# Performance work log

Hardware: AMD Instinct MI355X
Metric: run time of the kernel (lower is better)

The kernel has to match this reference:

```python
import jax, jax.numpy as jnp
import numpy as np

NUM_HEADS = 12

def rel_indices(N):
    # [N, N, 3] = (dx, dy, dist^2) between patches on an img x img grid
    img = int(N ** 0.5)
    ind = jnp.arange(img)[None, :] - jnp.arange(img)[:, None]      # [img, img]
    indx = jnp.tile(ind, (img, img))                               # [N, N]
    indy = jnp.repeat(jnp.repeat(ind, img, axis=0), img, axis=1)   # [N, N]
    indd = indx ** 2 + indy ** 2
    return jnp.stack([indx, indy, indd], axis=-1).astype(jnp.float32)

def setup_inputs() -> dict:
    key = jax.random.key(0)
    ks = jax.random.split(key, 8)
    B, N, C, H = 16, 576, 768, NUM_HEADS
    std = 0.02  # trunc_normal init scale in the original
    return {
        "x": jax.random.normal(ks[0], (B, N, C), jnp.float32),
        "w_qk": jax.random.normal(ks[1], (C, 2 * C), jnp.float32) * std,
        "w_v": jax.random.normal(ks[2], (C, C), jnp.float32) * std,
        "w_proj": jax.random.normal(ks[3], (C, C), jnp.float32) * std,
        "b_proj": jnp.zeros((C,), jnp.float32),
        "w_pos": jax.random.normal(ks[4], (3, H), jnp.float32) * std,
        "b_pos": jnp.zeros((H,), jnp.float32),
        "gating": jnp.ones((H,), jnp.float32),
    }

def reference(x, w_qk, w_v, w_proj, b_proj, w_pos, b_pos, gating):
    B, N, C = x.shape
    H = NUM_HEADS
    Dh = C // H
    scale = Dh ** -0.5

    # q, k: [B, H, N, Dh]
    qk = (x @ w_qk).reshape(B, N, 2, H, Dh)
    q = jnp.transpose(qk[:, :, 0], (0, 2, 1, 3))
    k = jnp.transpose(qk[:, :, 1], (0, 2, 1, 3))

    # content scores, softmax over keys
    patch_score = jax.nn.softmax(
        jnp.einsum("bhnd,bhmd->bhnm", q, k) * scale, axis=-1)

    # positional scores: rel_indices [N,N,3] -> [H,N,N], softmax over keys
    rel = rel_indices(N)
    pos_logits = jnp.einsum("nmk,kh->hnm", rel, w_pos) + b_pos[:, None, None]
    pos_score = jax.nn.softmax(pos_logits, axis=-1)  # [H, N, N]

    # sigmoid gating + renormalization
    g = jax.nn.sigmoid(gating)[None, :, None, None]
    attn = (1.0 - g) * patch_score + g * pos_score[None]
    attn = attn / jnp.sum(attn, axis=-1, keepdims=True)

    # v: [B, H, N, Dh]
    v = jnp.transpose((x @ w_v).reshape(B, N, H, Dh), (0, 2, 1, 3))

    out = jnp.einsum("bhnm,bhmd->bnhd", attn, v).reshape(B, N, C)
    out = out @ w_proj + b_proj
    return (out, attn, v)
```

## Files before the change

kernel.cpp:

```cpp
#include <hip/hip_runtime.h>
#include <hip/hip_bf16.h>

typedef __bf16 bf16;
typedef __attribute__((ext_vector_type(4))) __bf16 bf16x4;
typedef __attribute__((ext_vector_type(8))) __bf16 bf16x8;
typedef __attribute__((ext_vector_type(4))) float floatx4;

#define BB 16
#define NN 576
#define CC 768
#define HH 12
#define DH 64

#define GLOAD_LDS16(gp, lp) __builtin_amdgcn_global_load_lds( \
    (const __attribute__((address_space(1))) unsigned int*)(const void*)(gp), \
    (__attribute__((address_space(3))) unsigned int*)(void*)(lp), 16, 0, 0)

__global__ void k_convert(const float* __restrict__ in, bf16* __restrict__ out, int n4){
  int i = blockIdx.x*blockDim.x + threadIdx.x;
  if (i < n4){
    float4 f = ((const float4*)in)[i];
    bf16x4 o;
    o[0]=(bf16)f.x; o[1]=(bf16)f.y; o[2]=(bf16)f.z; o[3]=(bf16)f.w;
    ((bf16x4*)out)[i] = o;
  }
}

__global__ void k_transpose(const float* __restrict__ src, bf16* __restrict__ dst, int R, int Cc){
  __shared__ float tile[32][33];
  int c0 = blockIdx.x*32, r0 = blockIdx.y*32;
  int tx = threadIdx.x & 31, ty = threadIdx.x >> 5;
  #pragma unroll
  for (int i=0;i<4;i++)
    tile[ty + i*8][tx] = src[(size_t)(r0 + ty + i*8)*Cc + c0 + tx];
  __syncthreads();
  #pragma unroll
  for (int i=0;i<4;i++)
    dst[(size_t)(c0 + ty + i*8)*R + r0 + tx] = (bf16)tile[tx][ty + i*8];
}

__global__ __launch_bounds__(256) void k_pos(const float* __restrict__ w_pos, bf16* __restrict__ pos){
  int t = threadIdx.x, wv = t>>6, lane = t&63;
  int rowid = blockIdx.x*4 + wv;
  int h = rowid / NN, n = rowid % NN;
  float w0 = w_pos[h], w1 = w_pos[HH + h], w2 = w_pos[2*HH + h];
  int nx = n % 24, ny = n / 24;
  float e[9]; float mx = -1e30f;
  #pragma unroll
  for (int j=0;j<9;j++){
    int idx = lane + 64*j;
    int qq = idx / 144;
    int r  = idx - qq*144;
    int m  = (r>>2)*16 + qq*4 + (r&3);
    float dx = (float)(m % 24 - nx);
    float dy = (float)(m / 24 - ny);
    float l = dx*w0 + dy*w1 + (dx*dx + dy*dy)*w2;
    e[j] = l; mx = fmaxf(mx, l);
  }
  #pragma unroll
  for (int s=1;s<64;s<<=1) mx = fmaxf(mx, __shfl_xor(mx, s, 64));
  float sum = 0.f;
  #pragma unroll
  for (int j=0;j<9;j++){ e[j] = __expf(e[j]-mx); sum += e[j]; }
  #pragma unroll
  for (int s=1;s<64;s<<=1) sum += __shfl_xor(sum, s, 64);
  float inv = 1.f/sum;
  bf16* dst = pos + (size_t)rowid*NN;
  #pragma unroll
  for (int j=0;j<9;j++) dst[lane + 64*j] = (bf16)(e[j]*inv);
}

__device__ __forceinline__ void gemm128_main(
    const bf16* __restrict__ A, const bf16* __restrict__ B,
    int lda, int ldb, int K, bf16* As, bf16* Bs, floatx4 (*acc)[4])
{
  int t = threadIdx.x;
  int w = t>>6, m16 = t&15, q = (t&63)>>4;
  int wr = (w>>1)*64, wc = (w&1)*64;
  int sr = t>>2, kg = (t&3)*8;
  bf16* ldsA = As + w*512;
  bf16* ldsB = Bs + w*512;
  for (int k0 = 0; k0 < K; k0 += 32){
    GLOAD_LDS16(A + (size_t)sr*lda      + k0 + kg, ldsA);
    GLOAD_LDS16(A + (size_t)(sr+64)*lda + k0 + kg, ldsA + 2048);
    GLOAD_LDS16(B + (size_t)sr*ldb      + k0 + kg, ldsB);
    GLOAD_LDS16(B + (size_t)(sr+64)*ldb + k0 + kg, ldsB + 2048);
    __syncthreads();
    bf16x8 af[4], bfv[4];
    #pragma unroll
    for (int rt=0;rt<4;rt++) af[rt]  = *(const bf16x8*)&As[(wr + rt*16 + m16)*32 + q*8];
    #pragma unroll
    for (int ct=0;ct<4;ct++) bfv[ct] = *(const bf16x8*)&Bs[(wc + ct*16 + m16)*32 + q*8];
    #pragma unroll
    for (int rt=0;rt<4;rt++)
      #pragma unroll
      for (int ct=0;ct<4;ct++)
        acc[rt][ct] = __builtin_amdgcn_mfma_f32_16x16x32_bf16(af[rt], bfv[ct], acc[rt][ct], 0, 0, 0);
    __syncthreads();
  }
}

__global__ __launch_bounds__(256) void k_gemm1(
    const bf16* __restrict__ x_bf, const bf16* __restrict__ wcatT,
    bf16* __restrict__ q_bf, bf16* __restrict__ k_bf,
    bf16* __restrict__ vt_bf, float* __restrict__ v_out)
{
  __shared__ bf16 As[128*32];
  __shared__ bf16 Bs[128*32];
  int cb = blockIdx.x % 18, rb = blockIdx.x / 18;
  int rowBase = rb*128, colBase = cb*128;
  floatx4 zero = {0.f,0.f,0.f,0.f};
  floatx4 acc[4][4];
  #pragma unroll
  for (int a=0;a<4;a++)
    #pragma unroll
    for (int b=0;b<4;b++) acc[a][b] = zero;
  gemm128_main(x_bf + (size_t)rowBase*CC, wcatT + (size_t)colBase*CC, CC, CC, CC, As, Bs, acc);
  int t = threadIdx.x;
  int w = t>>6, m16 = t&15, q = (t&63)>>4;
  int wr = (w>>1)*64, wc = (w&1)*64;
  #pragma unroll
  for (int rt=0;rt<4;rt++){
    #pragma unroll
    for (int i=0;i<4;i++){
      int row = rowBase + wr + rt*16 + q*4 + i;
      int b = row / NN, n = row % NN;
      #pragma unroll
      for (int ct=0;ct<4;ct++){
        int col = colBase + wc + ct*16 + m16;
        float val = acc[rt][ct][i];
        if (col < 2*CC){
          int s = col / CC, rem = col % CC;
          int h = rem >> 6, d = rem & 63;
          bf16* dst = s ? k_bf : q_bf;
          float sv = s ? val : val*0.125f;
          dst[(((size_t)(b*HH + h)*NN + n) << 6) + d] = (bf16)sv;
        } else {
          int rem = col - 2*CC;
          int h = rem >> 6, d = rem & 63;
          v_out[(((size_t)(b*HH + h)*NN + n) << 6) + d] = val;
          vt_bf[((size_t)(b*HH + h)*DH + d)*NN + n] = (bf16)val;
        }
      }
    }
  }
}

__global__ __launch_bounds__(256, 2) void k_attn_pv(
    const bf16* __restrict__ q_bf, const bf16* __restrict__ k_bf,
    const bf16* __restrict__ vt_bf,
    const bf16* __restrict__ pos, const float* __restrict__ gating,
    float* __restrict__ attn_out, bf16* __restrict__ out1_bf)
{
  __shared__ __align__(16) char smem[64*1200];
  int qt = blockIdx.x % 9, bh = blockIdx.x / 9;
  int b = bh / HH, h = bh % HH;
  int n0 = qt*64;
  int t = threadIdx.x;
  int wv = t>>6, m16 = t&15, q = (t&63)>>4;

  const bf16* qrow = q_bf + ((size_t)bh*NN + n0 + wv*16 + m16)*DH;
  bf16x8 afr0 = *(const bf16x8*)&qrow[q*8];
  bf16x8 afr1 = *(const bf16x8*)&qrow[32 + q*8];

  const bf16* Kg = k_bf + (size_t)bh*NN*DH;
  floatx4 acc[36];
  #pragma unroll
  for (int T=0;T<36;T++) acc[T] = (floatx4){0.f,0.f,0.f,0.f};

  int key0 = t>>3, g16 = (t&7) ^ (key0 & 7);
  #pragma unroll
  for (int kt=0; kt<9; kt++){
    __syncthreads();
    const bf16* src0 = Kg + (size_t)(kt*64 + key0)*DH + g16*8;
    GLOAD_LDS16(src0,           smem + wv*1024);
    GLOAD_LDS16(src0 + 32*DH,   smem + 4096 + wv*1024);
    __syncthreads();
    #pragma unroll
    for (int ct=0; ct<4; ct++){
      int key = ct*16 + m16;
      int swz = key & 7;
      bf16x8 k0 = *(const bf16x8*)(smem + key*128 + ((q ^ swz)<<4));
      bf16x8 k1 = *(const bf16x8*)(smem + key*128 + (((4 + q) ^ swz)<<4));
      acc[kt*4+ct] = __builtin_amdgcn_mfma_f32_16x16x32_bf16(k0, afr0, acc[kt*4+ct], 0, 0, 0);
      acc[kt*4+ct] = __builtin_amdgcn_mfma_f32_16x16x32_bf16(k1, afr1, acc[kt*4+ct], 0, 0, 0);
    }
  }

  float mx = -1e30f;
  #pragma unroll
  for (int T=0;T<36;T++)
    #pragma unroll
    for (int i=0;i<4;i++) mx = fmaxf(mx, acc[T][i]);
  mx = fmaxf(mx, __shfl_xor(mx, 16, 64));
  mx = fmaxf(mx, __shfl_xor(mx, 32, 64));
  float ps = 0.f;
  #pragma unroll
  for (int T=0;T<36;T++)
    #pragma unroll
    for (int i=0;i<4;i++){ float e = __expf(acc[T][i]-mx); acc[T][i]=e; ps += e; }
  ps += __shfl_xor(ps, 16, 64);
  ps += __shfl_xor(ps, 32, 64);

  float g = 1.f/(1.f + __expf(-gating[h]));
  float ig = (1.f-g)/ps, bs = 0.f;

  const bf16* posrow = pos + ((size_t)h*NN + n0 + wv*16 + m16)*NN + q*144;
  #pragma unroll
  for (int T2=0;T2<18;T2++){
    bf16x8 pv = *(const bf16x8*)&posrow[T2*8];
    #pragma unroll
    for (int u=0;u<2;u++)
      #pragma unroll
      for (int i=0;i<4;i++){
        float a = ig*acc[T2*2+u][i] + g*(float)pv[u*4+i];
        acc[T2*2+u][i] = a; bs += a;
      }
  }
  bs += __shfl_xor(bs, 16, 64);
  bs += __shfl_xor(bs, 32, 64);
  float inv = 1.f/bs;

  __syncthreads();
  float* arow = attn_out + ((size_t)bh*NN + n0 + wv*16 + m16)*NN + q*4;
  char* prow = smem + (size_t)(wv*16 + m16)*1200 + q*8;
  #pragma unroll
  for (int T=0;T<36;T++){
    float4 o; bf16x4 pb;
    o.x = acc[T][0]*inv; o.y = acc[T][1]*inv; o.z = acc[T][2]*inv; o.w = acc[T][3]*inv;
    pb[0]=(bf16)o.x; pb[1]=(bf16)o.y; pb[2]=(bf16)o.z; pb[3]=(bf16)o.w;
    *(float4*)(arow + (size_t)T*16) = o;
    *(bf16x4*)(prow + T*32) = pb;
  }
  __syncthreads();

  floatx4 pacc[4];
  #pragma unroll
  for (int ct=0;ct<4;ct++) pacc[ct] = (floatx4){0.f,0.f,0.f,0.f};
  const char* pbase = smem + (size_t)(wv*16 + m16)*1200 + q*16;
  const bf16* vbase = vt_bf + (size_t)bh*DH*NN + q*8;
  #pragma unroll
  for (int c=0;c<18;c++){
    bf16x8 afr = *(const bf16x8*)(pbase + c*64);
    #pragma unroll
    for (int ct=0;ct<4;ct++){
      bf16x8 bfr = *(const bf16x8*)&vbase[(size_t)(ct*16+m16)*NN + c*32];
      pacc[ct] = __builtin_amdgcn_mfma_f32_16x16x32_bf16(afr, bfr, pacc[ct], 0, 0, 0);
    }
  }
  int rowq = n0 + wv*16 + q*4;
  bf16* obase = out1_bf + ((size_t)(b*NN + rowq))*CC + h*DH + m16;
  #pragma unroll
  for (int ct=0;ct<4;ct++)
    #pragma unroll
    for (int i=0;i<4;i++)
      obase[(size_t)i*CC + ct*16] = (bf16)pacc[ct][i];
}

__global__ __launch_bounds__(256) void k_proj(
    const bf16* __restrict__ out1_bf, const bf16* __restrict__ wprojT,
    const float* __restrict__ b_proj, float* __restrict__ out)
{
  __shared__ bf16 As[128*32];
  __shared__ bf16 Bs[128*32];
  int cb = blockIdx.x % 6, rb = blockIdx.x / 6;
  int rowBase = rb*128, colBase = cb*128;
  floatx4 zero = {0.f,0.f,0.f,0.f};
  floatx4 acc[4][4];
  #pragma unroll
  for (int a=0;a<4;a++)
    #pragma unroll
    for (int b=0;b<4;b++) acc[a][b] = zero;
  gemm128_main(out1_bf + (size_t)rowBase*CC, wprojT + (size_t)colBase*CC, CC, CC, CC, As, Bs, acc);
  int t = threadIdx.x;
  int w = t>>6, m16 = t&15, q = (t&63)>>4;
  int wr = (w>>1)*64, wc = (w&1)*64;
  #pragma unroll
  for (int rt=0;rt<4;rt++){
    #pragma unroll
    for (int i=0;i<4;i++){
      int row = rowBase + wr + rt*16 + q*4 + i;
      #pragma unroll
      for (int ct=0;ct<4;ct++){
        int col = colBase + wc + ct*16 + m16;
        out[(size_t)row*CC + col] = acc[rt][ct][i] + b_proj[col];
      }
    }
  }
}

extern "C" void kernel_launch(void* const* d_in, const int* in_sizes, int n_in,
                              void* d_out, int out_size, void* d_ws, size_t ws_size,
                              hipStream_t stream)
{
  (void)in_sizes; (void)n_in; (void)out_size; (void)ws_size;
  const float* x      = (const float*)d_in[0];
  const float* w_qk   = (const float*)d_in[1];
  const float* w_v    = (const float*)d_in[2];
  const float* w_proj = (const float*)d_in[3];
  const float* b_proj = (const float*)d_in[4];
  const float* w_pos  = (const float*)d_in[5];
  const float* gating = (const float*)d_in[7];

  float* out_ptr  = (float*)d_out;
  float* attn_ptr = out_ptr + (size_t)BB*NN*CC;
  float* v_ptr    = attn_ptr + (size_t)BB*HH*NN*NN;

  char* w = (char*)d_ws;
  bf16* x_bf    = (bf16*)(w);
  bf16* wcatT   = (bf16*)(w + 14155776);
  bf16* wprojT  = (bf16*)(w + 17694720);
  bf16* q_bf    = (bf16*)(w + 18874368);
  bf16* k_bf    = (bf16*)(w + 33030144);
  bf16* vt_bf   = (bf16*)(w + 47185920);
  bf16* pos_bf  = (bf16*)(w + 61341696);
  bf16* out1_bf = x_bf;

  k_convert<<<6912, 256, 0, stream>>>(x, x_bf, (BB*NN*CC)/4);
  k_transpose<<<dim3(48,24), 256, 0, stream>>>(w_qk, wcatT, CC, 2*CC);
  k_transpose<<<dim3(24,24), 256, 0, stream>>>(w_v, wcatT + (size_t)2*CC*CC, CC, CC);
  k_transpose<<<dim3(24,24), 256, 0, stream>>>(w_proj, wprojT, CC, CC);
  k_pos<<<(HH*NN)/4, 256, 0, stream>>>(w_pos, pos_bf);
  k_gemm1<<<72*18, 256, 0, stream>>>(x_bf, wcatT, q_bf, k_bf, vt_bf, v_ptr);
  k_attn_pv<<<192*9, 256, 0, stream>>>(q_bf, k_bf, vt_bf, pos_bf, gating, attn_ptr, out1_bf);
  k_proj<<<72*6, 256, 0, stream>>>(out1_bf, wprojT, b_proj, out_ptr);
}
```

Before: 543.5 us.

## Preload full K tile into LDS once and split PV work by V columns

Issues the whole per-head K block (576 keys x 64 dims, about 72KB) into LDS with async global-to-LDS loads at kernel start. This replaces nine load/sync rounds with one barrier and overlaps the loads with the Q fragment reads. The PV stage is also re-partitioned so each wave owns 16 output columns across all 64 rows, reading P from LDS and its own V slice once rather than loading all four V column tiles. The cost is a larger LDS footprint that is still inside the existing 75KB buffer, and each wave now reads P rows written by other waves.

```diff
diff --git a/kernel.cpp b/kernel.cpp
--- a/kernel.cpp
+++ b/kernel.cpp
@@ -159,31 +159,36 @@
   int t = threadIdx.x;
   int wv = t>>6, m16 = t&15, q = (t&63)>>4;
 
+  int key0 = t>>3, g16 = (t&7) ^ (key0 & 7);
+  const bf16* Kg = k_bf + (size_t)bh*NN*DH;
+  const bf16* ksrc = Kg + (size_t)key0*DH + g16*8;
+  char* kdst = smem + wv*1024;
+  #pragma unroll
+  for (int r=0;r<18;r++)
+    GLOAD_LDS16(ksrc + (size_t)(r*32)*DH, kdst + r*4096);
+
   const bf16* qrow = q_bf + ((size_t)bh*NN + n0 + wv*16 + m16)*DH;
-  bf16x8 afr0 = *(const bf16x8*)&qrow[q*8];
-  bf16x8 afr1 = *(const bf16x8*)&qrow[32 + q*8];
-
-  const bf16* Kg = k_bf + (size_t)bh*NN*DH;
+  bf16x8 qf0 = *(const bf16x8*)&qrow[q*8];
+  bf16x8 qf1 = *(const bf16x8*)&qrow[32 + q*8];
+  float gh = gating[h];
+
   floatx4 acc[36];
   #pragma unroll
   for (int T=0;T<36;T++) acc[T] = (floatx4){0.f,0.f,0.f,0.f};
 
-  int key0 = t>>3, g16 = (t&7) ^ (key0 & 7);
+  __syncthreads();
+
   #pragma unroll
   for (int kt=0; kt<9; kt++){
-    __syncthreads();
-    const bf16* src0 = Kg + (size_t)(kt*64 + key0)*DH + g16*8;
-    GLOAD_LDS16(src0,           smem + wv*1024);
-    GLOAD_LDS16(src0 + 32*DH,   smem + 4096 + wv*1024);
-    __syncthreads();
     #pragma unroll
     for (int ct=0; ct<4; ct++){
-      int key = ct*16 + m16;
+      int key = kt*64 + ct*16 + m16;
       int swz = key & 7;
-      bf16x8 k0 = *(const bf16x8*)(smem + key*128 + ((q ^ swz)<<4));
-      bf16x8 k1 = *(const bf16x8*)(smem + key*128 + (((4 + q) ^ swz)<<4));
-      acc[kt*4+ct] = __builtin_amdgcn_mfma_f32_16x16x32_bf16(k0, afr0, acc[kt*4+ct], 0, 0, 0);
-      acc[kt*4+ct] = __builtin_amdgcn_mfma_f32_16x16x32_bf16(k1, afr1, acc[kt*4+ct], 0, 0, 0);
+      const char* kb = smem + (size_t)key*128;
+      bf16x8 k0 = *(const bf16x8*)(kb + ((q ^ swz)<<4));
+      bf16x8 k1 = *(const bf16x8*)(kb + (((4 + q) ^ swz)<<4));
+      acc[kt*4+ct] = __builtin_amdgcn_mfma_f32_16x16x32_bf16(k0, qf0, acc[kt*4+ct], 0, 0, 0);
+      acc[kt*4+ct] = __builtin_amdgcn_mfma_f32_16x16x32_bf16(k1, qf1, acc[kt*4+ct], 0, 0, 0);
     }
   }
 
@@ -202,7 +207,7 @@
   ps += __shfl_xor(ps, 16, 64);
   ps += __shfl_xor(ps, 32, 64);
 
-  float g = 1.f/(1.f + __expf(-gating[h]));
+  float g = 1.f/(1.f + __expf(-gh));
   float ig = (1.f-g)/ps, bs = 0.f;
 
   const bf16* posrow = pos + ((size_t)h*NN + n0 + wv*16 + m16)*NN + q*144;
@@ -236,25 +241,23 @@
 
   floatx4 pacc[4];
   #pragma unroll
-  for (int ct=0;ct<4;ct++) pacc[ct] = (floatx4){0.f,0.f,0.f,0.f};
-  const char* pbase = smem + (size_t)(wv*16 + m16)*1200 + q*16;
-  const bf16* vbase = vt_bf + (size_t)bh*DH*NN + q*8;
+  for (int rt=0;rt<4;rt++) pacc[rt] = (floatx4){0.f,0.f,0.f,0.f};
+  const bf16* vb = vt_bf + (size_t)bh*DH*NN + (size_t)(wv*16 + m16)*NN + q*8;
   #pragma unroll
   for (int c=0;c<18;c++){
-    bf16x8 afr = *(const bf16x8*)(pbase + c*64);
-    #pragma unroll
-    for (int ct=0;ct<4;ct++){
-      bf16x8 bfr = *(const bf16x8*)&vbase[(size_t)(ct*16+m16)*NN + c*32];
-      pacc[ct] = __builtin_amdgcn_mfma_f32_16x16x32_bf16(afr, bfr, pacc[ct], 0, 0, 0);
+    bf16x8 bfr = *(const bf16x8*)&vb[c*32];
+    #pragma unroll
+    for (int rt=0;rt<4;rt++){
+      bf16x8 afr = *(const bf16x8*)(smem + (size_t)(rt*16 + m16)*1200 + q*16 + c*64);
+      pacc[rt] = __builtin_amdgcn_mfma_f32_16x16x32_bf16(afr, bfr, pacc[rt], 0, 0, 0);
     }
   }
-  int rowq = n0 + wv*16 + q*4;
-  bf16* obase = out1_bf + ((size_t)(b*NN + rowq))*CC + h*DH + m16;
-  #pragma unroll
-  for (int ct=0;ct<4;ct++)
+  bf16* ob = out1_bf + ((size_t)(b*NN + n0))*CC + h*DH + wv*16 + m16;
+  #pragma unroll
+  for (int rt=0;rt<4;rt++)
     #pragma unroll
     for (int i=0;i<4;i++)
-      obase[(size_t)i*CC + ct*16] = (bf16)pacc[ct][i];
+      ob[(size_t)(rt*16 + q*4 + i)*CC] = (bf16)pacc[rt][i];
 }
 
 __global__ __launch_bounds__(256) void k_proj(
```

Measured after the change: 520.7 us. -4.2%, faster.
